# Optimization experiments

Measured on AMD Instinct MI355X. Metric: run time of the kernel, lower is better.

## Reference

```python
import jax, jax.numpy as jnp
import numpy as np

N, E, IN, H, OUT, G = 100000, 1600000, 9, 64, 6, 1024
EPS = 1e-5


def setup_inputs() -> dict:
    key = jax.random.key(0)
    ks = jax.random.split(key, 24)
    inp = {
        "x": jax.random.normal(ks[0], (N, IN), dtype=jnp.float32),
        "edge_index": jax.random.randint(ks[1], (2, E), 0, N, dtype=jnp.int64),
        "edge_weight": jax.random.uniform(ks[2], (E,), dtype=jnp.float32),
        "batch": jnp.sort(jax.random.randint(ks[3], (N,), 0, G, dtype=jnp.int64)),
    }
    def lin(k, fan_in, fan_out):
        return jax.random.normal(k, (fan_in, fan_out), dtype=jnp.float32) / np.sqrt(fan_in)
    # GraphConv layer 0: IN -> H; layers 1,2: H -> H
    inp["W_rel0"], inp["W_root0"], inp["b0"] = lin(ks[4], IN, H), lin(ks[5], IN, H), jnp.zeros((H,), jnp.float32)
    inp["W_rel1"], inp["W_root1"], inp["b1"] = lin(ks[6], H, H), lin(ks[7], H, H), jnp.zeros((H,), jnp.float32)
    inp["W_rel2"], inp["W_root2"], inp["b2"] = lin(ks[8], H, H), lin(ks[9], H, H), jnp.zeros((H,), jnp.float32)
    # BatchNorm params for the first num_layers-1 = 2 layers
    inp["g0"], inp["be0"] = jnp.ones((H,), jnp.float32), jnp.zeros((H,), jnp.float32)
    inp["g1"], inp["be1"] = jnp.ones((H,), jnp.float32), jnp.zeros((H,), jnp.float32)
    # MLP head
    inp["W_l1"], inp["b_l1"] = lin(ks[10], H, H), jnp.zeros((H,), jnp.float32)
    inp["W_l2"], inp["b_l2"] = lin(ks[11], H, OUT), jnp.zeros((OUT,), jnp.float32)
    return inp


def graph_conv(x, src, dst, ew, W_rel, W_root, b):
    # PyG GraphConv: out = aggr_add(e_ji * x_j) @ W_rel + b + x @ W_root
    msg = x[src] * ew[:, None]                      # [E, F] gather
    agg = jax.ops.segment_sum(msg, dst, num_segments=x.shape[0])  # [N, F] scatter-add
    return agg @ W_rel + b + x @ W_root


def batch_norm(x, g, b):
    m = jnp.mean(x, axis=0)
    v = jnp.var(x, axis=0)
    return (x - m) * jax.lax.rsqrt(v + EPS) * g + b


def reference(x, edge_index, edge_weight, batch,
              W_rel0, W_root0, b0, W_rel1, W_root1, b1, W_rel2, W_root2, b2,
              g0, be0, g1, be1, W_l1, b_l1, W_l2, b_l2):
    src, dst = edge_index[0], edge_index[1]
    # layer 0: conv -> BN -> relu (dropout p applied only in training; eval here)
    h = graph_conv(x, src, dst, edge_weight, W_rel0, W_root0, b0)
    h = jax.nn.relu(batch_norm(h, g0, be0))
    # layer 1
    h = graph_conv(h, src, dst, edge_weight, W_rel1, W_root1, b1)
    h = jax.nn.relu(batch_norm(h, g1, be1))
    # layer 2 (no norm/relu)
    h = graph_conv(h, src, dst, edge_weight, W_rel2, W_root2, b2)
    # global mean pool over graphs
    summed = jax.ops.segment_sum(h, batch, num_segments=G)            # [G, H]
    counts = jax.ops.segment_sum(jnp.ones((h.shape[0],), h.dtype), batch, num_segments=G)
    pooled = summed / jnp.maximum(counts, 1.0)[:, None]
    # MLP head
    z = jax.nn.relu(pooled @ W_l1 + b_l1)
    return z @ W_l2 + b_l2
```

## Files before the change

### kernel.cpp

```cpp
#include <hip/hip_runtime.h>
#include <hip/hip_fp16.h>

constexpr int N    = 100000;
constexpr int E    = 1600000;
constexpr int FIN  = 9;
constexpr int OUTF = 6;
constexpr int G    = 1024;
constexpr int NPB  = 256;
constexpr int NB   = (N + NPB - 1) / NPB;
constexpr int CH   = 2048;
constexpr int NCH  = (E + CH - 1) / CH;
constexpr int BCAP = 4864;
constexpr int CBCAP= BCAP + NPB + 8;
constexpr int EBUF = 5888;
constexpr int ZCNT = 256 + G * 64;

typedef _Float16 f16x8 __attribute__((ext_vector_type(8)));
typedef float    f32x4 __attribute__((ext_vector_type(4)));

__device__ __forceinline__ void atomAddF(float* p, float v) { unsafeAtomicAdd(p, v); }

__global__ __launch_bounds__(256) void initK(int* __restrict__ cursor, float* __restrict__ zeros,
    const float* __restrict__ x, __half* __restrict__ x9)
{
    int i = blockIdx.x * 256 + threadIdx.x;
    if (i < NB) cursor[i] = i * BCAP;
    if (i < ZCNT) zeros[i] = 0.f;
    if (i < N * FIN) x9[i] = __float2half(x[i]);
}

__global__ __launch_bounds__(256) void passA(const int* __restrict__ src, const int* __restrict__ dst,
    const float* __restrict__ ew, int* __restrict__ cursor, int2* __restrict__ bucketed)
{
    __shared__ int h[NB];
    __shared__ int hb[NB];
    int t = threadIdx.x;
    for (int i = t; i < NB; i += 256) h[i] = 0;
    __syncthreads();
    int base = blockIdx.x * CH;
    int myS[8], myD[8], rk[8]; float myW[8];
#pragma unroll
    for (int i = 0; i < 8; i++) {
        int e = base + i * 256 + t;
        if (e < E) {
            myS[i] = src[e]; myD[i] = dst[e]; myW[i] = ew[e];
            rk[i] = atomicAdd(&h[myD[i] >> 8], 1);
        } else myD[i] = -1;
    }
    __syncthreads();
    for (int i = t; i < NB; i += 256) hb[i] = h[i] ? atomicAdd(&cursor[i], h[i]) : 0;
    __syncthreads();
#pragma unroll
    for (int i = 0; i < 8; i++) if (myD[i] >= 0) {
        int packed = myS[i] | ((myD[i] & 255) << 24);
        bucketed[hb[myD[i] >> 8] + rk[i]] = make_int2(packed, __float_as_int(myW[i]));
    }
}

__global__ __launch_bounds__(NPB) void passB(const int* __restrict__ cursor,
    const int2* __restrict__ bucketed, int* __restrict__ ebeg, int* __restrict__ eend,
    int2* __restrict__ csr)
{
    __shared__ int2 ebuf[EBUF];
    __shared__ int cl[NPB], sa[NPB], sb[NPB], curs[NPB];
    int b = blockIdx.x, t = threadIdx.x;
    int node0 = b * NPB;
    int nnode = min(NPB, N - node0);
    int cnt = cursor[b] - b * BCAP;
    int abase = b * BCAP;
    int base = b * CBCAP;
    bool fits = (cnt <= EBUF);
    cl[t] = 0;
    __syncthreads();
    for (int e = t; e < cnt; e += NPB) {
        int2 r = bucketed[abase + e];
        if (fits) ebuf[e] = r;
        atomicAdd(&cl[((unsigned)r.x) >> 24], 1);
    }
    __syncthreads();
    int deg = cl[t];
    int pc = (deg + 1) & ~1;
    int* cur = sa; int* nxt = sb;
    cur[t] = pc;
    __syncthreads();
    for (int o = 1; o < NPB; o <<= 1) {
        int v = cur[t];
        if (t >= o) v += cur[t - o];
        nxt[t] = v;
        __syncthreads();
        int* tmp = cur; cur = nxt; nxt = tmp;
    }
    int off = cur[t] - pc;
    if (t < nnode) { ebeg[node0 + t] = base + off; eend[node0 + t] = base + off + deg; }
    curs[t] = off;
    __syncthreads();
    for (int e = t; e < cnt; e += NPB) {
        int2 r = fits ? ebuf[e] : bucketed[abase + e];
        int dl = ((unsigned)r.x) >> 24;
        int pos = base + atomicAdd(&curs[dl], 1);
        csr[pos] = make_int2(r.x & 0x00FFFFFF, r.y);
    }
    __syncthreads();
    if (t < nnode && (deg & 1)) csr[base + off + deg] = make_int2(0, 0);
    if (t < 4) csr[base + cur[NPB - 1] + t] = make_int2(0, 0);
}

__global__ __launch_bounds__(256) void wprep(const float* __restrict__ Wrel1, const float* __restrict__ Wroot1,
    const float* __restrict__ Wrel2, const float* __restrict__ Wroot2, __half* __restrict__ Wt)
{
    int i = blockIdx.x * 256 + threadIdx.x;
    int layer = i >> 13, r = i & 8191;
    int c = r >> 6, k = r & 63;
    const float* Wrel = layer ? Wrel2 : Wrel1;
    const float* Wroot = layer ? Wroot2 : Wroot1;
    float v = (c < 64) ? Wrel[k * 64 + c] : Wroot[k * 64 + (c - 64)];
    Wt[i] = __float2half(v);
}

__global__ __launch_bounds__(256) void g9proj(const __half* __restrict__ x9,
    const int2* __restrict__ csr, const int* __restrict__ ebeg, const int* __restrict__ eend,
    const float* __restrict__ x, const float* __restrict__ Wrel, const float* __restrict__ Wroot,
    const float* __restrict__ bias, __half* __restrict__ H0, float* __restrict__ stats)
{
    int t = threadIdx.x, lane = t & 63;
    int es = lane >> 4, fc = min(lane & 15, FIN - 1);
    float wrel[FIN], wroot[FIN];
#pragma unroll
    for (int k = 0; k < FIN; k++) { wrel[k] = Wrel[k * 64 + lane]; wroot[k] = Wroot[k * 64 + lane]; }
    float bj = bias[lane];
    float s1 = 0.f, s2 = 0.f;
    int wv = (blockIdx.x * blockDim.x + t) >> 6;
    int nw = (gridDim.x * blockDim.x) >> 6;
    for (int n = wv; n < N; n += nw) {
        int beg = ebeg[n], end = eend[n];
        int last = end - 1;
        int2 eA0 = csr[min(beg + es,      last)];
        int2 eB0 = csr[min(beg + 4 + es,  last)];
        int2 eA1 = csr[min(beg + 8 + es,  last)];
        int2 eB1 = csr[min(beg + 12 + es, last)];
        __half xA = x9[(size_t)eA0.x * FIN + fc];
        __half xB = x9[(size_t)eB0.x * FIN + fc];
        float a0 = 0.f, a1 = 0.f;
        for (int k = beg; k < end; k += 8) {
            int2 eA2 = csr[min(k + 16 + es, last)];
            int2 eB2 = csr[min(k + 20 + es, last)];
            __half nxA = x9[(size_t)eA1.x * FIN + fc];
            __half nxB = x9[(size_t)eB1.x * FIN + fc];
            float wA = (k + es     < end) ? __int_as_float(eA0.y) : 0.f;
            float wB = (k + 4 + es < end) ? __int_as_float(eB0.y) : 0.f;
            a0 = fmaf(wA, __half2float(xA), a0);
            a1 = fmaf(wB, __half2float(xB), a1);
            eA0 = eA1; eB0 = eB1; eA1 = eA2; eB1 = eB2;
            xA = nxA; xB = nxB;
        }
        float r = a0 + a1;
        r += __shfl(r, lane ^ 16, 64);
        r += __shfl(r, lane ^ 32, 64);
        float h = bj;
#pragma unroll
        for (int k2 = 0; k2 < FIN; k2++) {
            float ak = __shfl(r, k2, 64);
            h = fmaf(ak, wrel[k2], h);
            h = fmaf(x[(size_t)n * FIN + k2], wroot[k2], h);
        }
        H0[(size_t)n * 64 + lane] = __float2half(h);
        s1 += h; s2 += h * h;
    }
    __shared__ float sred[256];
    sred[t] = s1; __syncthreads();
    if (t < 64) atomAddF(&stats[t], sred[t] + sred[t+64] + sred[t+128] + sred[t+192]);
    __syncthreads();
    sred[t] = s2; __syncthreads();
    if (t < 64) atomAddF(&stats[64 + t], sred[t] + sred[t+64] + sred[t+128] + sred[t+192]);
}

__global__ __launch_bounds__(256) void projm(const __half* __restrict__ Hin, const __half* __restrict__ Wt,
    const float* __restrict__ bias, const float* __restrict__ stats,
    const float* __restrict__ gam, const float* __restrict__ bet,
    __half* __restrict__ P, __half* __restrict__ Hout)
{
    int t = threadIdx.x, lane = t & 63;
    int wv = blockIdx.x * 4 + (t >> 6);
    int nw = gridDim.x * 4;
    int n16 = lane & 15, quad = lane >> 4;
    constexpr float invN = 1.0f / (float)N;
    float sc[16], sh[16];
#pragma unroll
    for (int jj = 0; jj < 16; jj++) {
        int k = (jj < 8) ? (quad * 8 + jj) : (32 + quad * 8 + (jj - 8));
        float m = stats[k] * invN;
        float v = stats[64 + k] * invN - m * m;
        sc[jj] = gam[k] * rsqrtf(v + 1e-5f);
        sh[jj] = bet[k] - m * sc[jj];
    }
    f16x8 bf[8][2];
#pragma unroll
    for (int ct = 0; ct < 8; ct++)
#pragma unroll
        for (int kh = 0; kh < 2; kh++)
            bf[ct][kh] = *(const f16x8*)(Wt + (size_t)(ct * 16 + n16) * 64 + kh * 32 + quad * 8);
    float bcol[4];
#pragma unroll
    for (int i = 0; i < 4; i++) bcol[i] = bias[i * 16 + n16];
    const int NT = N / 16;
    for (int tile = wv; tile < NT; tile += nw) {
        int n0 = tile * 16;
        f16x8 r0 = *(const f16x8*)(Hin + (size_t)(n0 + n16) * 64 + quad * 8);
        f16x8 r1 = *(const f16x8*)(Hin + (size_t)(n0 + n16) * 64 + 32 + quad * 8);
        f16x8 a0, a1;
#pragma unroll
        for (int jj = 0; jj < 8; jj++) {
            a0[jj] = (_Float16)fmaxf(fmaf((float)r0[jj], sc[jj],     sh[jj]),     0.f);
            a1[jj] = (_Float16)fmaxf(fmaf((float)r1[jj], sc[jj + 8], sh[jj + 8]), 0.f);
        }
        f32x4 acc[8];
#pragma unroll
        for (int ct = 0; ct < 8; ct++) {
            f32x4 c = {0.f, 0.f, 0.f, 0.f};
            c = __builtin_amdgcn_mfma_f32_16x16x32_f16(a0, bf[ct][0], c, 0, 0, 0);
            c = __builtin_amdgcn_mfma_f32_16x16x32_f16(a1, bf[ct][1], c, 0, 0, 0);
            acc[ct] = c;
        }
#pragma unroll
        for (int ct = 0; ct < 8; ct++) {
#pragma unroll
            for (int r = 0; r < 4; r++) {
                int n = n0 + quad * 4 + r;
                if (ct < 4) P[(size_t)n * 64 + ct * 16 + n16] = __float2half(acc[ct][r]);
                else Hout[(size_t)n * 64 + (ct - 4) * 16 + n16] = __float2half(acc[ct][r] + bcol[ct - 4]);
            }
        }
    }
}

template<int EPI>
__global__ __launch_bounds__(256) void gather(const __half* __restrict__ P, __half* H,
    const int2* __restrict__ csr, const int* __restrict__ ebeg, const int* __restrict__ eend,
    float* __restrict__ stats, const int* __restrict__ batch, float* __restrict__ pool)
{
    int t = threadIdx.x, lane = t & 63;
    int wv = (blockIdx.x * blockDim.x + t) >> 6;
    int nw = (gridDim.x * blockDim.x) >> 6;
    float s1 = 0.f, s2 = 0.f;
    const int NPAIR = N / 2;
    for (int pr = wv; pr < NPAIR; pr += nw) {
        int n0 = 2 * pr, n1 = n0 + 1;
        int b0 = ebeg[n0], m0 = (eend[n0] - b0 + 1) >> 1;
        int b1 = ebeg[n1], m1 = (eend[n1] - b1 + 1) >> 1;
        const int4* q0 = (const int4*)csr + (b0 >> 1);
        const int4* q1 = (const int4*)csr + (b1 >> 1);
        int c0 = max(m0 - 1, 0), c1 = max(m1 - 1, 0);
        float x0 = __half2float(H[(size_t)n0 * 64 + lane]);
        float x1 = __half2float(H[(size_t)n1 * 64 + lane]);
        int mm = max(m0, m1);
        int4 qa = q0[0], qb = q0[min(1, c0)], qc = q1[0], qd = q1[min(1, c1)];
        __half v0a0 = P[(size_t)qa.x * 64 + lane], v0a1 = P[(size_t)qa.z * 64 + lane];
        __half v0b0 = P[(size_t)qb.x * 64 + lane], v0b1 = P[(size_t)qb.z * 64 + lane];
        __half v0c0 = P[(size_t)qc.x * 64 + lane], v0c1 = P[(size_t)qc.z * 64 + lane];
        __half v0d0 = P[(size_t)qd.x * 64 + lane], v0d1 = P[(size_t)qd.z * 64 + lane];
        float w0a = (0 < m0) ? __int_as_float(qa.y) : 0.f, w0A = (0 < m0) ? __int_as_float(qa.w) : 0.f;
        float w0b = (1 < m0) ? __int_as_float(qb.y) : 0.f, w0B = (1 < m0) ? __int_as_float(qb.w) : 0.f;
        float w0c = (0 < m1) ? __int_as_float(qc.y) : 0.f, w0C = (0 < m1) ? __int_as_float(qc.w) : 0.f;
        float w0d = (1 < m1) ? __int_as_float(qd.y) : 0.f, w0D = (1 < m1) ? __int_as_float(qd.w) : 0.f;
        qa = q0[min(2, c0)]; qb = q0[min(3, c0)]; qc = q1[min(2, c1)]; qd = q1[min(3, c1)];
        __half v1a0 = P[(size_t)qa.x * 64 + lane], v1a1 = P[(size_t)qa.z * 64 + lane];
        __half v1b0 = P[(size_t)qb.x * 64 + lane], v1b1 = P[(size_t)qb.z * 64 + lane];
        __half v1c0 = P[(size_t)qc.x * 64 + lane], v1c1 = P[(size_t)qc.z * 64 + lane];
        __half v1d0 = P[(size_t)qd.x * 64 + lane], v1d1 = P[(size_t)qd.z * 64 + lane];
        float w1a = (2 < m0) ? __int_as_float(qa.y) : 0.f, w1A = (2 < m0) ? __int_as_float(qa.w) : 0.f;
        float w1b = (3 < m0) ? __int_as_float(qb.y) : 0.f, w1B = (3 < m0) ? __int_as_float(qb.w) : 0.f;
        float w1c = (2 < m1) ? __int_as_float(qc.y) : 0.f, w1C = (2 < m1) ? __int_as_float(qc.w) : 0.f;
        float w1d = (3 < m1) ? __int_as_float(qd.y) : 0.f, w1D = (3 < m1) ? __int_as_float(qd.w) : 0.f;
        int4 Qa = q0[min(4, c0)], Qb = q0[min(5, c0)], Qc = q1[min(4, c1)], Qd = q1[min(5, c1)];
        float a0 = 0.f, a1 = 0.f, a2 = 0.f, a3 = 0.f;
        float a4 = 0.f, a5 = 0.f, a6 = 0.f, a7 = 0.f;
        for (int k = 0; k < mm; k += 2) {
            int4 Na = q0[min(k + 6, c0)], Nb = q0[min(k + 7, c0)];
            int4 Nc = q1[min(k + 6, c1)], Nd = q1[min(k + 7, c1)];
            __half v2a0 = P[(size_t)Qa.x * 64 + lane], v2a1 = P[(size_t)Qa.z * 64 + lane];
            __half v2b0 = P[(size_t)Qb.x * 64 + lane], v2b1 = P[(size_t)Qb.z * 64 + lane];
            __half v2c0 = P[(size_t)Qc.x * 64 + lane], v2c1 = P[(size_t)Qc.z * 64 + lane];
            __half v2d0 = P[(size_t)Qd.x * 64 + lane], v2d1 = P[(size_t)Qd.z * 64 + lane];
            float w2a = (k + 4 < m0) ? __int_as_float(Qa.y) : 0.f, w2A = (k + 4 < m0) ? __int_as_float(Qa.w) : 0.f;
            float w2b = (k + 5 < m0) ? __int_as_float(Qb.y) : 0.f, w2B = (k + 5 < m0) ? __int_as_float(Qb.w) : 0.f;
            float w2c = (k + 4 < m1) ? __int_as_float(Qc.y) : 0.f, w2C = (k + 4 < m1) ? __int_as_float(Qc.w) : 0.f;
            float w2d = (k + 5 < m1) ? __int_as_float(Qd.y) : 0.f, w2D = (k + 5 < m1) ? __int_as_float(Qd.w) : 0.f;
            a0 = fmaf(w0a, __half2float(v0a0), a0); a1 = fmaf(w0A, __half2float(v0a1), a1);
            a2 = fmaf(w0b, __half2float(v0b0), a2); a3 = fmaf(w0B, __half2float(v0b1), a3);
            a4 = fmaf(w0c, __half2float(v0c0), a4); a5 = fmaf(w0C, __half2float(v0c1), a5);
            a6 = fmaf(w0d, __half2float(v0d0), a6); a7 = fmaf(w0D, __half2float(v0d1), a7);
            w0a = w1a; w0A = w1A; w0b = w1b; w0B = w1B; w0c = w1c; w0C = w1C; w0d = w1d; w0D = w1D;
            w1a = w2a; w1A = w2A; w1b = w2b; w1B = w2B; w1c = w2c; w1C = w2C; w1d = w2d; w1D = w2D;
            v0a0 = v1a0; v0a1 = v1a1; v0b0 = v1b0; v0b1 = v1b1;
            v0c0 = v1c0; v0c1 = v1c1; v0d0 = v1d0; v0d1 = v1d1;
            v1a0 = v2a0; v1a1 = v2a1; v1b0 = v2b0; v1b1 = v2b1;
            v1c0 = v2c0; v1c1 = v2c1; v1d0 = v2d0; v1d1 = v2d1;
            Qa = Na; Qb = Nb; Qc = Nc; Qd = Nd;
        }
        float r0 = x0 + ((a0 + a2) + (a1 + a3));
        float r1 = x1 + ((a4 + a6) + (a5 + a7));
        if constexpr (EPI == 0) {
            H[(size_t)n0 * 64 + lane] = __float2half(r0);
            H[(size_t)n1 * 64 + lane] = __float2half(r1);
            s1 += r0 + r1; s2 += r0 * r0 + r1 * r1;
        } else {
            atomAddF(&pool[batch[n0] * 64 + lane], r0);
            atomAddF(&pool[batch[n1] * 64 + lane], r1);
        }
    }
    if constexpr (EPI == 0) {
        __shared__ float sred[256];
        sred[t] = s1; __syncthreads();
        if (t < 64) atomAddF(&stats[t], sred[t] + sred[t+64] + sred[t+128] + sred[t+192]);
        __syncthreads();
        sred[t] = s2; __syncthreads();
        if (t < 64) atomAddF(&stats[64 + t], sred[t] + sred[t+64] + sred[t+128] + sred[t+192]);
    }
}

__global__ __launch_bounds__(64) void head(const float* __restrict__ pool,
    const int* __restrict__ batch, const float* __restrict__ Wl1, const float* __restrict__ bl1,
    const float* __restrict__ Wl2, const float* __restrict__ bl2, float* __restrict__ out)
{
    int g = blockIdx.x, t = threadIdx.x;
    __shared__ float sp[64];
    __shared__ float sz[64];
    __shared__ int scnt;
    if (t == 0) {
        int lo = 0, hi = N;
        while (lo < hi) { int m = (lo + hi) >> 1; if (batch[m] < g) lo = m + 1; else hi = m; }
        int lo2 = lo, hi2 = N;
        while (lo2 < hi2) { int m = (lo2 + hi2) >> 1; if (batch[m] < g + 1) lo2 = m + 1; else hi2 = m; }
        scnt = lo2 - lo;
    }
    __syncthreads();
    float cnt = fmaxf((float)scnt, 1.0f);
    sp[t] = pool[g * 64 + t] / cnt;
    __syncthreads();
    float acc = bl1[t];
#pragma unroll
    for (int k = 0; k < 64; k++) acc = fmaf(sp[k], Wl1[k * 64 + t], acc);
    sz[t] = fmaxf(acc, 0.f);
    __syncthreads();
    if (t < OUTF) {
        float o = bl2[t];
#pragma unroll
        for (int k = 0; k < 64; k++) o = fmaf(sz[k], Wl2[k * OUTF + t], o);
        out[g * OUTF + t] = o;
    }
}

extern "C" void kernel_launch(void* const* d_in, const int* in_sizes, int n_in,
                              void* d_out, int out_size, void* d_ws, size_t ws_size,
                              hipStream_t stream)
{
    const float* x     = (const float*)d_in[0];
    const int*   ei    = (const int*)d_in[1];
    const float* ew    = (const float*)d_in[2];
    const int*   batch = (const int*)d_in[3];
    const float* Wrel0 = (const float*)d_in[4];
    const float* Wroot0= (const float*)d_in[5];
    const float* b0    = (const float*)d_in[6];
    const float* Wrel1 = (const float*)d_in[7];
    const float* Wroot1= (const float*)d_in[8];
    const float* b1    = (const float*)d_in[9];
    const float* Wrel2 = (const float*)d_in[10];
    const float* Wroot2= (const float*)d_in[11];
    const float* b2    = (const float*)d_in[12];
    const float* g0    = (const float*)d_in[13];
    const float* be0   = (const float*)d_in[14];
    const float* g1    = (const float*)d_in[15];
    const float* be1   = (const float*)d_in[16];
    const float* Wl1   = (const float*)d_in[17];
    const float* bl1   = (const float*)d_in[18];
    const float* Wl2   = (const float*)d_in[19];
    const float* bl2   = (const float*)d_in[20];
    const int* srcI = ei;
    const int* dstI = ei + E;

    __half* Ha     = (__half*)d_ws;
    __half* Hb     = Ha + (size_t)N * 64;
    __half* P      = Hb + (size_t)N * 64;
    int2*   csr    = (int2*)(P + (size_t)N * 64);
    int*    ebeg   = (int*)(csr + (size_t)NB * CBCAP);
    int*    eend   = ebeg + N;
    int*    cursor = eend + N;
    float*  stats0 = (float*)(cursor + NB);
    float*  stats1 = stats0 + 128;
    float*  pool   = stats1 + 128;
    __half* Wt1    = (__half*)(pool + G * 64);
    __half* Wt2    = Wt1 + 128 * 64;
    __half* x9     = Wt2 + 128 * 64;
    int2*   bucketed = (int2*)Ha;

    initK<<<(N * FIN + 255) / 256, 256, 0, stream>>>(cursor, stats0, x, x9);
    passA<<<NCH, 256, 0, stream>>>(srcI, dstI, ew, cursor, bucketed);
    passB<<<NB, NPB, 0, stream>>>(cursor, bucketed, ebeg, eend, csr);
    wprep<<<64, 256, 0, stream>>>(Wrel1, Wroot1, Wrel2, Wroot2, Wt1);

    g9proj<<<2048, 256, 0, stream>>>(x9, csr, ebeg, eend, x, Wrel0, Wroot0, b0, Ha, stats0);

    projm<<<1024, 256, 0, stream>>>(Ha, Wt1, b1, stats0, g0, be0, P, Hb);
    gather<0><<<2048, 256, 0, stream>>>(P, Hb, csr, ebeg, eend, stats1, nullptr, nullptr);

    projm<<<1024, 256, 0, stream>>>(Hb, Wt2, b2, stats1, g1, be1, P, Ha);
    gather<1><<<2048, 256, 0, stream>>>(P, Ha, csr, ebeg, eend, nullptr, batch, pool);

    head<<<G, 64, 0, stream>>>(pool, batch, Wl1, bl1, Wl2, bl2, (float*)d_out);
}
```

Baseline: 485.3 us.

## Replace per-node-pair gather with edge-parallel block gather into shared tile

The gather kernels now assign each block a contiguous range of 64 destination nodes and split that block's CSR edge range evenly across waves. Each wave scatters weighted messages into a shared-memory accumulator tile with LDS atomics, using the local destination index kept in the high byte of the CSR source field. This is meant to remove load imbalance and wasted lanes caused by variable per-node degree in the old node-pair loop. The cost is LDS atomic contention, a 16 KB shared tile per block, and keeping the destination byte in the CSR, which g9proj now masks out.

```diff
diff --git a/kernel.cpp b/kernel.cpp
--- a/kernel.cpp
+++ b/kernel.cpp
@@ -14,6 +14,7 @@
 constexpr int CBCAP= BCAP + NPB + 8;
 constexpr int EBUF = 5888;
 constexpr int ZCNT = 256 + G * 64;
+constexpr int NBK64= (N + 63) / 64;
 
 typedef _Float16 f16x8 __attribute__((ext_vector_type(8)));
 typedef float    f32x4 __attribute__((ext_vector_type(4)));
@@ -98,10 +99,10 @@
         int2 r = fits ? ebuf[e] : bucketed[abase + e];
         int dl = ((unsigned)r.x) >> 24;
         int pos = base + atomicAdd(&curs[dl], 1);
-        csr[pos] = make_int2(r.x & 0x00FFFFFF, r.y);
-    }
-    __syncthreads();
-    if (t < nnode && (deg & 1)) csr[base + off + deg] = make_int2(0, 0);
+        csr[pos] = make_int2(r.x, r.y);
+    }
+    __syncthreads();
+    if (t < nnode && (deg & 1)) csr[base + off + deg] = make_int2(t << 24, 0);
     if (t < 4) csr[base + cur[NPB - 1] + t] = make_int2(0, 0);
 }
 
@@ -138,14 +139,14 @@
         int2 eB0 = csr[min(beg + 4 + es,  last)];
         int2 eA1 = csr[min(beg + 8 + es,  last)];
         int2 eB1 = csr[min(beg + 12 + es, last)];
-        __half xA = x9[(size_t)eA0.x * FIN + fc];
-        __half xB = x9[(size_t)eB0.x * FIN + fc];
+        __half xA = x9[(size_t)(eA0.x & 0x00FFFFFF) * FIN + fc];
+        __half xB = x9[(size_t)(eB0.x & 0x00FFFFFF) * FIN + fc];
         float a0 = 0.f, a1 = 0.f;
         for (int k = beg; k < end; k += 8) {
             int2 eA2 = csr[min(k + 16 + es, last)];
             int2 eB2 = csr[min(k + 20 + es, last)];
-            __half nxA = x9[(size_t)eA1.x * FIN + fc];
-            __half nxB = x9[(size_t)eB1.x * FIN + fc];
+            __half nxA = x9[(size_t)(eA1.x & 0x00FFFFFF) * FIN + fc];
+            __half nxB = x9[(size_t)(eB1.x & 0x00FFFFFF) * FIN + fc];
             float wA = (k + es     < end) ? __int_as_float(eA0.y) : 0.f;
             float wB = (k + 4 + es < end) ? __int_as_float(eB0.y) : 0.f;
             a0 = fmaf(wA, __half2float(xA), a0);
@@ -234,78 +235,78 @@
 }
 
 template<int EPI>
-__global__ __launch_bounds__(256) void gather(const __half* __restrict__ P, __half* H,
+__global__ __launch_bounds__(256) void gatherE(const __half* __restrict__ P, __half* __restrict__ H,
     const int2* __restrict__ csr, const int* __restrict__ ebeg, const int* __restrict__ eend,
     float* __restrict__ stats, const int* __restrict__ batch, float* __restrict__ pool)
 {
-    int t = threadIdx.x, lane = t & 63;
-    int wv = (blockIdx.x * blockDim.x + t) >> 6;
-    int nw = (gridDim.x * blockDim.x) >> 6;
+    __shared__ float tile[64 * 64];
+    int t = threadIdx.x, lane = t & 63, wave = t >> 6;
+    int n0 = blockIdx.x * 64;
+    int nend = min(n0 + 64, N);
+    int qoff = n0 & 255;
+    for (int i = t; i < 64 * 64; i += 256) tile[i] = 0.f;
+    int pbeg = ebeg[n0];
+    int pend = (eend[nend - 1] + 1) & ~1;
+    __syncthreads();
+    const int4* csr4 = (const int4*)csr;
+    int i4max = (pend >> 1) - 1;
+
+    if (pend > pbeg) {
+        int k0 = pbeg + wave * 8;
+        int4 A0, A1, A2, A3, B0, B1, B2, B3;
+        __half vA[8]; float wA[8]; int dA[8];
+        {
+            int b4 = k0 >> 1;
+            A0 = csr4[min(b4,     i4max)]; A1 = csr4[min(b4 + 1, i4max)];
+            A2 = csr4[min(b4 + 2, i4max)]; A3 = csr4[min(b4 + 3, i4max)];
+            b4 = (k0 + 32) >> 1;
+            B0 = csr4[min(b4,     i4max)]; B1 = csr4[min(b4 + 1, i4max)];
+            B2 = csr4[min(b4 + 2, i4max)]; B3 = csr4[min(b4 + 3, i4max)];
+            int xs[8] = {A0.x, A0.z, A1.x, A1.z, A2.x, A2.z, A3.x, A3.z};
+            int ys[8] = {A0.y, A0.w, A1.y, A1.w, A2.y, A2.w, A3.y, A3.w};
+#pragma unroll
+            for (int j = 0; j < 8; j++) {
+                vA[j] = P[(size_t)(xs[j] & 0x00FFFFFF) * 64 + lane];
+                wA[j] = (k0 + j < pend) ? __int_as_float(ys[j]) : 0.f;
+                dA[j] = (int)(((unsigned)xs[j]) >> 24) - qoff;
+            }
+        }
+        for (int k = k0; k < pend; k += 32) {
+            int b4 = (k + 64) >> 1;
+            int4 C0 = csr4[min(b4,     i4max)], C1 = csr4[min(b4 + 1, i4max)];
+            int4 C2 = csr4[min(b4 + 2, i4max)], C3 = csr4[min(b4 + 3, i4max)];
+            int xs[8] = {B0.x, B0.z, B1.x, B1.z, B2.x, B2.z, B3.x, B3.z};
+            int ys[8] = {B0.y, B0.w, B1.y, B1.w, B2.y, B2.w, B3.y, B3.w};
+            __half vB[8]; float wB[8]; int dB[8];
+#pragma unroll
+            for (int j = 0; j < 8; j++) {
+                vB[j] = P[(size_t)(xs[j] & 0x00FFFFFF) * 64 + lane];
+                wB[j] = (k + 32 + j < pend) ? __int_as_float(ys[j]) : 0.f;
+                dB[j] = (int)(((unsigned)xs[j]) >> 24) - qoff;
+            }
+#pragma unroll
+            for (int j = 0; j < 8; j++)
+                atomicAdd(&tile[dA[j] * 64 + lane], wA[j] * __half2float(vA[j]));
+            A0 = B0; A1 = B1; A2 = B2; A3 = B3;
+            B0 = C0; B1 = C1; B2 = C2; B3 = C3;
+#pragma unroll
+            for (int j = 0; j < 8; j++) { vA[j] = vB[j]; wA[j] = wB[j]; dA[j] = dB[j]; }
+        }
+    }
+    __syncthreads();
     float s1 = 0.f, s2 = 0.f;
-    const int NPAIR = N / 2;
-    for (int pr = wv; pr < NPAIR; pr += nw) {
-        int n0 = 2 * pr, n1 = n0 + 1;
-        int b0 = ebeg[n0], m0 = (eend[n0] - b0 + 1) >> 1;
-        int b1 = ebeg[n1], m1 = (eend[n1] - b1 + 1) >> 1;
-        const int4* q0 = (const int4*)csr + (b0 >> 1);
-        const int4* q1 = (const int4*)csr + (b1 >> 1);
-        int c0 = max(m0 - 1, 0), c1 = max(m1 - 1, 0);
-        float x0 = __half2float(H[(size_t)n0 * 64 + lane]);
-        float x1 = __half2float(H[(size_t)n1 * 64 + lane]);
-        int mm = max(m0, m1);
-        int4 qa = q0[0], qb = q0[min(1, c0)], qc = q1[0], qd = q1[min(1, c1)];
-        __half v0a0 = P[(size_t)qa.x * 64 + lane], v0a1 = P[(size_t)qa.z * 64 + lane];
-        __half v0b0 = P[(size_t)qb.x * 64 + lane], v0b1 = P[(size_t)qb.z * 64 + lane];
-        __half v0c0 = P[(size_t)qc.x * 64 + lane], v0c1 = P[(size_t)qc.z * 64 + lane];
-        __half v0d0 = P[(size_t)qd.x * 64 + lane], v0d1 = P[(size_t)qd.z * 64 + lane];
-        float w0a = (0 < m0) ? __int_as_float(qa.y) : 0.f, w0A = (0 < m0) ? __int_as_float(qa.w) : 0.f;
-        float w0b = (1 < m0) ? __int_as_float(qb.y) : 0.f, w0B = (1 < m0) ? __int_as_float(qb.w) : 0.f;
-        float w0c = (0 < m1) ? __int_as_float(qc.y) : 0.f, w0C = (0 < m1) ? __int_as_float(qc.w) : 0.f;
-        float w0d = (1 < m1) ? __int_as_float(qd.y) : 0.f, w0D = (1 < m1) ? __int_as_float(qd.w) : 0.f;
-        qa = q0[min(2, c0)]; qb = q0[min(3, c0)]; qc = q1[min(2, c1)]; qd = q1[min(3, c1)];
-        __half v1a0 = P[(size_t)qa.x * 64 + lane], v1a1 = P[(size_t)qa.z * 64 + lane];
-        __half v1b0 = P[(size_t)qb.x * 64 + lane], v1b1 = P[(size_t)qb.z * 64 + lane];
-        __half v1c0 = P[(size_t)qc.x * 64 + lane], v1c1 = P[(size_t)qc.z * 64 + lane];
-        __half v1d0 = P[(size_t)qd.x * 64 + lane], v1d1 = P[(size_t)qd.z * 64 + lane];
-        float w1a = (2 < m0) ? __int_as_float(qa.y) : 0.f, w1A = (2 < m0) ? __int_as_float(qa.w) : 0.f;
-        float w1b = (3 < m0) ? __int_as_float(qb.y) : 0.f, w1B = (3 < m0) ? __int_as_float(qb.w) : 0.f;
-        float w1c = (2 < m1) ? __int_as_float(qc.y) : 0.f, w1C = (2 < m1) ? __int_as_float(qc.w) : 0.f;
-        float w1d = (3 < m1) ? __int_as_float(qd.y) : 0.f, w1D = (3 < m1) ? __int_as_float(qd.w) : 0.f;
-        int4 Qa = q0[min(4, c0)], Qb = q0[min(5, c0)], Qc = q1[min(4, c1)], Qd = q1[min(5, c1)];
-        float a0 = 0.f, a1 = 0.f, a2 = 0.f, a3 = 0.f;
-        float a4 = 0.f, a5 = 0.f, a6 = 0.f, a7 = 0.f;
-        for (int k = 0; k < mm; k += 2) {
-            int4 Na = q0[min(k + 6, c0)], Nb = q0[min(k + 7, c0)];
-            int4 Nc = q1[min(k + 6, c1)], Nd = q1[min(k + 7, c1)];
-            __half v2a0 = P[(size_t)Qa.x * 64 + lane], v2a1 = P[(size_t)Qa.z * 64 + lane];
-            __half v2b0 = P[(size_t)Qb.x * 64 + lane], v2b1 = P[(size_t)Qb.z * 64 + lane];
-            __half v2c0 = P[(size_t)Qc.x * 64 + lane], v2c1 = P[(size_t)Qc.z * 64 + lane];
-            __half v2d0 = P[(size_t)Qd.x * 64 + lane], v2d1 = P[(size_t)Qd.z * 64 + lane];
-            float w2a = (k + 4 < m0) ? __int_as_float(Qa.y) : 0.f, w2A = (k + 4 < m0) ? __int_as_float(Qa.w) : 0.f;
-            float w2b = (k + 5 < m0) ? __int_as_float(Qb.y) : 0.f, w2B = (k + 5 < m0) ? __int_as_float(Qb.w) : 0.f;
-            float w2c = (k + 4 < m1) ? __int_as_float(Qc.y) : 0.f, w2C = (k + 4 < m1) ? __int_as_float(Qc.w) : 0.f;
-            float w2d = (k + 5 < m1) ? __int_as_float(Qd.y) : 0.f, w2D = (k + 5 < m1) ? __int_as_float(Qd.w) : 0.f;
-            a0 = fmaf(w0a, __half2float(v0a0), a0); a1 = fmaf(w0A, __half2float(v0a1), a1);
-            a2 = fmaf(w0b, __half2float(v0b0), a2); a3 = fmaf(w0B, __half2float(v0b1), a3);
-            a4 = fmaf(w0c, __half2float(v0c0), a4); a5 = fmaf(w0C, __half2float(v0c1), a5);
-            a6 = fmaf(w0d, __half2float(v0d0), a6); a7 = fmaf(w0D, __half2float(v0d1), a7);
-            w0a = w1a; w0A = w1A; w0b = w1b; w0B = w1B; w0c = w1c; w0C = w1C; w0d = w1d; w0D = w1D;
-            w1a = w2a; w1A = w2A; w1b = w2b; w1B = w2B; w1c = w2c; w1C = w2C; w1d = w2d; w1D = w2D;
-            v0a0 = v1a0; v0a1 = v1a1; v0b0 = v1b0; v0b1 = v1b1;
-            v0c0 = v1c0; v0c1 = v1c1; v0d0 = v1d0; v0d1 = v1d1;
-            v1a0 = v2a0; v1a1 = v2a1; v1b0 = v2b0; v1b1 = v2b1;
-            v1c0 = v2c0; v1c1 = v2c1; v1d0 = v2d0; v1d1 = v2d1;
-            Qa = Na; Qb = Nb; Qc = Nc; Qd = Nd;
-        }
-        float r0 = x0 + ((a0 + a2) + (a1 + a3));
-        float r1 = x1 + ((a4 + a6) + (a5 + a7));
-        if constexpr (EPI == 0) {
-            H[(size_t)n0 * 64 + lane] = __float2half(r0);
-            H[(size_t)n1 * 64 + lane] = __float2half(r1);
-            s1 += r0 + r1; s2 += r0 * r0 + r1 * r1;
-        } else {
-            atomAddF(&pool[batch[n0] * 64 + lane], r0);
-            atomAddF(&pool[batch[n1] * 64 + lane], r1);
+#pragma unroll
+    for (int i = 0; i < 16; i++) {
+        int nl = wave * 16 + i;
+        int n = n0 + nl;
+        if (n < N) {
+            float h = __half2float(H[(size_t)n * 64 + lane]) + tile[nl * 64 + lane];
+            if constexpr (EPI == 0) {
+                H[(size_t)n * 64 + lane] = __float2half(h);
+                s1 += h; s2 += h * h;
+            } else {
+                atomAddF(&pool[batch[n] * 64 + lane], h);
+            }
         }
     }
     if constexpr (EPI == 0) {
@@ -401,10 +402,10 @@
     g9proj<<<2048, 256, 0, stream>>>(x9, csr, ebeg, eend, x, Wrel0, Wroot0, b0, Ha, stats0);
 
     projm<<<1024, 256, 0, stream>>>(Ha, Wt1, b1, stats0, g0, be0, P, Hb);
-    gather<0><<<2048, 256, 0, stream>>>(P, Hb, csr, ebeg, eend, stats1, nullptr, nullptr);
+    gatherE<0><<<NBK64, 256, 0, stream>>>(P, Hb, csr, ebeg, eend, stats1, nullptr, nullptr);
 
     projm<<<1024, 256, 0, stream>>>(Hb, Wt2, b2, stats1, g1, be1, P, Ha);
-    gather<1><<<2048, 256, 0, stream>>>(P, Ha, csr, ebeg, eend, nullptr, batch, pool);
+    gatherE<1><<<NBK64, 256, 0, stream>>>(P, Ha, csr, ebeg, eend, nullptr, batch, pool);
 
     head<<<G, 64, 0, stream>>>(pool, batch, Wl1, bl1, Wl2, bl2, (float*)d_out);
 }
```

Measured after the change: 1.540 ms. 3.17x slower.
